# Performance work log

Hardware: AMD Instinct MI355X
Metric: run time of the kernel (lower is better)

Reference implementation:

```python
import jax, jax.numpy as jnp
import numpy as np

D_CH = 2048  # channels
N = 64       # hidden_state
L = 8192     # sequence length
MIN_DELTA, MAX_DELTA = 1e-3, 0.1


def setup_inputs() -> dict:
    key = jax.random.key(0)
    ks = jax.random.split(key, 5)
    X = jax.random.normal(ks[0], (D_CH, L), jnp.float32)
    # kaiming_normal_(nonlinearity='linear'): std = 1/sqrt(fan_in=N)
    A = jax.random.normal(ks[1], (N, N), jnp.float32) * (1.0 / N) ** 0.5
    B = jax.random.normal(ks[2], (N, D_CH), jnp.float32) * (1.0 / N) ** 0.5
    C = jax.random.normal(ks[3], (D_CH, N), jnp.float32)
    Dp = jnp.ones((D_CH,), jnp.float32)
    log_delta = jax.random.uniform(ks[4], (1,), jnp.float32,
                                   float(np.log(MIN_DELTA)), float(np.log(MAX_DELTA)))
    return {"X": X, "A": A, "B": B, "C": C, "Dp": Dp, "log_delta": log_delta}


def reference(X, A, B, C, Dp, log_delta):
    # X: (D, L). Bilinear (Tustin) discretization with dt = exp(log_delta).
    n = A.shape[0]
    delta = jnp.exp(log_delta)[0]
    I = jnp.eye(n, dtype=A.dtype)
    inv = jnp.linalg.inv(I - (delta * 0.5) * A)
    dA = inv @ (I + (delta * 0.5) * A)      # (N, N)
    dB = delta * (inv @ B)                   # (N, D)

    def step(h, x_t):
        # h: (N,), x_t: (D,)
        h = dA @ h + dB @ x_t
        return h, C @ h                      # y_t: (D,)

    h0 = jnp.zeros((n,), X.dtype)
    _, ys = jax.lax.scan(step, h0, X.T)      # ys: (L, D)
    # skip connection y += D * X (per-channel)
    return ys.T + Dp[:, None] * X            # (D, L)
```

## Files before the change

kernel.cpp:

```cpp
#include <hip/hip_runtime.h>
#include <math.h>

#define D_CH 2048
#define LSEQ 8192
#define T1 32
#define NC1 256
#define VSLAB 524288

typedef __attribute__((ext_vector_type(8))) short bf16x8;
typedef __attribute__((ext_vector_type(4))) float f32x4;

__device__ __forceinline__ short f2bf(float x) {
  unsigned u = __float_as_uint(x);
  u += 0x7FFFu + ((u >> 16) & 1);
  return (short)(u >> 16);
}

__device__ __forceinline__ void mmzero(float acc[16]) {
#pragma unroll
  for (int t = 0; t < 16; ++t) acc[t] = 0.f;
}

template <int SZ>
__device__ __forceinline__ void mmld(float acc[16], const float* __restrict__ Z,
                                     int r0, int c0) {
#pragma unroll
  for (int i = 0; i < 4; ++i) {
    float4 z = *(const float4*)&Z[(r0 + i) * SZ + c0];
    acc[i * 4 + 0] = z.x; acc[i * 4 + 1] = z.y;
    acc[i * 4 + 2] = z.z; acc[i * 4 + 3] = z.w;
  }
}

template <int SX, int SY>
__device__ __forceinline__ void mac44(float acc[16], const float* __restrict__ Xb,
                                      const float* __restrict__ Yb, int r0, int c0) {
#pragma unroll 4
  for (int k = 0; k < 64; k += 4) {
    float4 x0 = *(const float4*)&Xb[(r0 + 0) * SX + k];
    float4 x1 = *(const float4*)&Xb[(r0 + 1) * SX + k];
    float4 x2 = *(const float4*)&Xb[(r0 + 2) * SX + k];
    float4 x3 = *(const float4*)&Xb[(r0 + 3) * SX + k];
    float4 y0 = *(const float4*)&Yb[(k + 0) * SY + c0];
    float4 y1 = *(const float4*)&Yb[(k + 1) * SY + c0];
    float4 y2 = *(const float4*)&Yb[(k + 2) * SY + c0];
    float4 y3 = *(const float4*)&Yb[(k + 3) * SY + c0];
#define MROW(i, xi) \
    acc[i * 4 + 0] += xi.x * y0.x + xi.y * y1.x + xi.z * y2.x + xi.w * y3.x; \
    acc[i * 4 + 1] += xi.x * y0.y + xi.y * y1.y + xi.z * y2.y + xi.w * y3.y; \
    acc[i * 4 + 2] += xi.x * y0.z + xi.y * y1.z + xi.z * y2.z + xi.w * y3.z; \
    acc[i * 4 + 3] += xi.x * y0.w + xi.y * y1.w + xi.z * y2.w + xi.w * y3.w;
    MROW(0, x0) MROW(1, x1) MROW(2, x2) MROW(3, x3)
#undef MROW
  }
}

template <int SZ>
__device__ __forceinline__ void mmst(float* Dst, const float acc[16], int r0, int c0) {
#pragma unroll
  for (int i = 0; i < 4; ++i)
    *(float4*)&Dst[(r0 + i) * SZ + c0] =
        make_float4(acc[i * 4 + 0], acc[i * 4 + 1], acc[i * 4 + 2], acc[i * 4 + 3]);
}

__global__ __launch_bounds__(256) void main_kernel(const float* __restrict__ X,
                                                   const float* __restrict__ A,
                                                   const float* __restrict__ B,
                                                   const float* __restrict__ logd,
                                                   float* __restrict__ invdT,
                                                   float* __restrict__ dAg,
                                                   float* __restrict__ V,
                                                   int KS) {
  __shared__ float smem[13056];
  const int tid = threadIdx.x;
  const int lane = tid & 63;
  const int w = tid >> 6;

  if (blockIdx.x == 0) {
    float* b0 = smem;
    float* b1 = smem + 4352;
    float* b2 = smem + 8704;
    const int r0 = (tid >> 4) * 4, c0 = (tid & 15) * 4;
    const float delta = expf(logd[0]);
    const float half = 0.5f * delta;
    float acc[16], acc2[16];

    for (int idx = tid; idx < 4096; idx += 256) {
      int i = idx >> 6, j = idx & 63;
      float p = half * A[idx];
      b0[i * 68 + j] = p;
      b2[i * 68 + j] = p + (i == j ? 1.f : 0.f);
    }
    __syncthreads();
    mmzero(acc); mac44<68, 68>(acc, b0, b0, r0, c0); mmst<68>(b1, acc, r0, c0);
    __syncthreads();
    mmld<68>(acc, b2, r0, c0); mac44<68, 68>(acc, b1, b2, r0, c0);
    mmzero(acc2); mac44<68, 68>(acc2, b1, b1, r0, c0);
    __syncthreads();
    mmst<68>(b0, acc, r0, c0); mmst<68>(b2, acc2, r0, c0);
    __syncthreads();
    mmld<68>(acc, b0, r0, c0); mac44<68, 68>(acc, b2, b0, r0, c0);
    mmzero(acc2); mac44<68, 68>(acc2, b2, b2, r0, c0);
    __syncthreads();
    mmst<68>(b1, acc, r0, c0); mmst<68>(b2, acc2, r0, c0);
    __syncthreads();
    mmld<68>(acc, b1, r0, c0); mac44<68, 68>(acc, b2, b1, r0, c0);
    __syncthreads();
    mmst<68>(b0, acc, r0, c0);
    __syncthreads();

    for (int idx = tid; idx < 4096; idx += 256) {
      int n = idx >> 6, m = idx & 63;
      float qv = b0[n * 68 + m];
      invdT[m * 64 + n] = delta * qv;
      dAg[idx] = 2.f * qv - (n == m ? 1.f : 0.f);
    }
    return;
  }

  const int b = blockIdx.x - 1;
  const int t0 = (b & 127) << 6;
  const int slab = b >> 7;
  const int k0 = slab * KS;
  short* Xs = (short*)smem;
  short* Bs = (short*)smem + 4608;
  const int q = lane >> 4, r = lane & 15;

  f32x4 acc[4];
#pragma unroll
  for (int j = 0; j < 4; ++j) acc[j] = (f32x4){0.f, 0.f, 0.f, 0.f};

  const int brow = (lane >> 3);
  const int bkc = (lane & 7) * 8;

  for (int kk = 0; kk < KS; kk += 64) {
    float xv[16];
    float bv[16];
#pragma unroll
    for (int p = 0; p < 2; ++p)
#pragma unroll
      for (int j = 0; j < 8; ++j)
        xv[p * 8 + j] = X[(size_t)(k0 + kk + p * 32 + w * 8 + j) * LSEQ + t0 + lane];
#pragma unroll
    for (int p = 0; p < 2; ++p) {
      int n = p * 32 + w * 8 + brow;
      float4 f0 = *(const float4*)&B[(size_t)n * D_CH + k0 + kk + bkc];
      float4 f1 = *(const float4*)&B[(size_t)n * D_CH + k0 + kk + bkc + 4];
      bv[p * 8 + 0] = f0.x; bv[p * 8 + 1] = f0.y; bv[p * 8 + 2] = f0.z; bv[p * 8 + 3] = f0.w;
      bv[p * 8 + 4] = f1.x; bv[p * 8 + 5] = f1.y; bv[p * 8 + 6] = f1.z; bv[p * 8 + 7] = f1.w;
    }
    __syncthreads();
#pragma unroll
    for (int p = 0; p < 2; ++p) {
      bf16x8 xp, bp;
#pragma unroll
      for (int j = 0; j < 8; ++j) { xp[j] = f2bf(xv[p * 8 + j]); bp[j] = f2bf(bv[p * 8 + j]); }
      *(bf16x8*)&Xs[lane * 72 + p * 32 + w * 8] = xp;
      *(bf16x8*)&Bs[(p * 32 + w * 8 + brow) * 72 + bkc] = bp;
    }
    __syncthreads();
#pragma unroll
    for (int ks = 0; ks < 64; ks += 32) {
      bf16x8 a = *(const bf16x8*)&Xs[(w * 16 + r) * 72 + ks + q * 8];
#pragma unroll
      for (int j = 0; j < 4; ++j) {
        bf16x8 bb = *(const bf16x8*)&Bs[(j * 16 + r) * 72 + ks + q * 8];
        acc[j] = __builtin_amdgcn_mfma_f32_16x16x32_bf16(a, bb, acc[j], 0, 0, 0);
      }
    }
  }
  float* Vs = V + (size_t)slab * VSLAB;
#pragma unroll
  for (int j = 0; j < 4; ++j)
#pragma unroll
    for (int reg = 0; reg < 4; ++reg)
      Vs[(size_t)(t0 + w * 16 + q * 4 + reg) * 64 + j * 16 + r] = acc[j][reg];
}

__device__ __forceinline__ float matvec(const float ar[64], const float* __restrict__ hb,
                                        float u) {
  float a0 = u, a1 = 0.f, a2 = 0.f, a3 = 0.f;
#pragma unroll
  for (int jj = 0; jj < 64; jj += 4) {
    float4 hv = *(const float4*)&hb[jj];
    a0 += ar[jj + 0] * hv.x;
    a1 += ar[jj + 1] * hv.y;
    a2 += ar[jj + 2] * hv.z;
    a3 += ar[jj + 3] * hv.w;
  }
  return (a0 + a1) + (a2 + a3);
}

__global__ __launch_bounds__(256) void scan1_kernel(const float* __restrict__ V,
                                                    const float* __restrict__ invdT,
                                                    const float* __restrict__ dA,
                                                    float* __restrict__ U,
                                                    float* __restrict__ S,
                                                    float* __restrict__ dA32g,
                                                    float* __restrict__ dA512g,
                                                    int nslab) {
  __shared__ float smem[8704];
  const int tid = threadIdx.x;
  const int c = blockIdx.x;

  if (c == NC1) {
    float* b0 = smem;
    float* b1 = smem + 4352;
    const int r0 = (tid >> 4) * 4, c0 = (tid & 15) * 4;
    for (int idx = tid; idx < 4096; idx += 256)
      b0[(idx >> 6) * 68 + (idx & 63)] = dA[idx];
    __syncthreads();
    float acc[16];
    float* p = b0; float* q = b1;
    for (int s = 1; s <= 9; ++s) {
      mmzero(acc); mac44<68, 68>(acc, p, p, r0, c0);
      if (s == 5) mmst<64>(dA32g, acc, r0, c0);
      if (s == 9) mmst<64>(dA512g, acc, r0, c0);
      mmst<68>(q, acc, r0, c0);
      __syncthreads();
      float* t = p; p = q; q = t;
    }
    return;
  }

  float* invs = smem;
  float* Vs   = smem + 4096;
  float* Us   = smem + 6144;
  float* hs0  = smem + 8192;
  float* hs1  = smem + 8256;

  for (int idx = tid; idx < 4096; idx += 256) invs[idx] = invdT[idx];
  for (int idx = tid; idx < 2048; idx += 256) {
    float v = 0.f;
    for (int s = 0; s < nslab; ++s) v += V[(size_t)s * VSLAB + (size_t)c * 2048 + idx];
    Vs[idx] = v;
  }
  __syncthreads();

  const int r0 = (tid >> 4) * 2, c0 = (tid & 15) * 4;
  float a0[4] = {0.f, 0.f, 0.f, 0.f}, a1[4] = {0.f, 0.f, 0.f, 0.f};
#pragma unroll 4
  for (int k = 0; k < 64; k += 4) {
    float4 v0 = *(const float4*)&Vs[r0 * 64 + k];
    float4 v1 = *(const float4*)&Vs[(r0 + 1) * 64 + k];
    float4 y0 = *(const float4*)&invs[(k + 0) * 64 + c0];
    float4 y1 = *(const float4*)&invs[(k + 1) * 64 + c0];
    float4 y2 = *(const float4*)&invs[(k + 2) * 64 + c0];
    float4 y3 = *(const float4*)&invs[(k + 3) * 64 + c0];
    a0[0] += v0.x * y0.x + v0.y * y1.x + v0.z * y2.x + v0.w * y3.x;
    a0[1] += v0.x * y0.y + v0.y * y1.y + v0.z * y2.y + v0.w * y3.y;
    a0[2] += v0.x * y0.z + v0.y * y1.z + v0.z * y2.z + v0.w * y3.z;
    a0[3] += v0.x * y0.w + v0.y * y1.w + v0.z * y2.w + v0.w * y3.w;
    a1[0] += v1.x * y0.x + v1.y * y1.x + v1.z * y2.x + v1.w * y3.x;
    a1[1] += v1.x * y0.y + v1.y * y1.y + v1.z * y2.y + v1.w * y3.y;
    a1[2] += v1.x * y0.z + v1.y * y1.z + v1.z * y2.z + v1.w * y3.z;
    a1[3] += v1.x * y0.w + v1.y * y1.w + v1.z * y2.w + v1.w * y3.w;
  }
  *(float4*)&Us[r0 * 64 + c0] = make_float4(a0[0], a0[1], a0[2], a0[3]);
  *(float4*)&Us[(r0 + 1) * 64 + c0] = make_float4(a1[0], a1[1], a1[2], a1[3]);
  *(float4*)&U[(size_t)(c * 32 + r0) * 64 + c0] = make_float4(a0[0], a0[1], a0[2], a0[3]);
  *(float4*)&U[(size_t)(c * 32 + r0 + 1) * 64 + c0] = make_float4(a1[0], a1[1], a1[2], a1[3]);
  __syncthreads();

  if (tid < 64) {
    float ar[64];
#pragma unroll
    for (int jj = 0; jj < 64; jj += 4) {
      float4 v = *(const float4*)&dA[tid * 64 + jj];
      ar[jj] = v.x; ar[jj + 1] = v.y; ar[jj + 2] = v.z; ar[jj + 3] = v.w;
    }
    float h = 0.f;
    hs0[tid] = 0.f;
    for (int t = 0; t < T1; ++t) {
      float u = Us[t * 64 + tid];
      h = matvec(ar, (t & 1) ? hs1 : hs0, u);
      ((t & 1) ? hs0 : hs1)[tid] = h;
    }
    S[c * 64 + tid] = h;
  }
}

__global__ __launch_bounds__(1024, 4) void mid_kernel(const float* __restrict__ S,
                                                      const float* __restrict__ dA32,
                                                      const float* __restrict__ dA512,
                                                      float* __restrict__ Hinit) {
  __shared__ float S2s[1024];
  __shared__ float H2s[1024];
  __shared__ float hsbuf[2048];
  const int tid = threadIdx.x;
  const int wave = tid >> 6, lane = tid & 63;
  float* hs0 = &hsbuf[wave * 128];
  float* hs1 = hs0 + 64;
  const float* inw = S + wave * 16 * 64;

  {
    float ar[64];
#pragma unroll
    for (int jj = 0; jj < 64; jj += 4) {
      float4 v = *(const float4*)&dA32[lane * 64 + jj];
      ar[jj] = v.x; ar[jj + 1] = v.y; ar[jj + 2] = v.z; ar[jj + 3] = v.w;
    }
    float h = 0.f;
    hs0[lane] = 0.f;
    for (int t = 0; t < 16; ++t) {
      float u = inw[t * 64 + lane];
      h = matvec(ar, (t & 1) ? hs1 : hs0, u);
      ((t & 1) ? hs0 : hs1)[lane] = h;
    }
    S2s[wave * 64 + lane] = h;
  }
  __syncthreads();

  if (wave == 0) {
    float br[64];
#pragma unroll
    for (int jj = 0; jj < 64; jj += 4) {
      float4 v = *(const float4*)&dA512[lane * 64 + jj];
      br[jj] = v.x; br[jj + 1] = v.y; br[jj + 2] = v.z; br[jj + 3] = v.w;
    }
    float g = 0.f;
    hs0[lane] = 0.f;
    for (int t = 0; t < 16; ++t) {
      H2s[t * 64 + lane] = g;
      float u = S2s[t * 64 + lane];
      g = matvec(br, (t & 1) ? hs1 : hs0, u);
      ((t & 1) ? hs0 : hs1)[lane] = g;
    }
  }
  __syncthreads();

  {
    float ar[64];
#pragma unroll
    for (int jj = 0; jj < 64; jj += 4) {
      float4 v = *(const float4*)&dA32[lane * 64 + jj];
      ar[jj] = v.x; ar[jj + 1] = v.y; ar[jj + 2] = v.z; ar[jj + 3] = v.w;
    }
    float h = H2s[wave * 64 + lane];
    hs0[lane] = h;
    for (int t = 0; t < 16; ++t) {
      Hinit[(wave * 16 + t) * 64 + lane] = h;
      float u = inw[t * 64 + lane];
      h = matvec(ar, (t & 1) ? hs1 : hs0, u);
      ((t & 1) ? hs0 : hs1)[lane] = h;
    }
  }
}

__global__ __launch_bounds__(64) void scan2_kernel(const float* __restrict__ U,
                                                   const float* __restrict__ dA,
                                                   const float* __restrict__ Hinit,
                                                   float* __restrict__ Ht) {
  __shared__ float hs[2][64];
  const int tid = threadIdx.x;
  const int c = blockIdx.x;
  float ar[64];
#pragma unroll
  for (int jj = 0; jj < 64; jj += 4) {
    float4 v = *(const float4*)&dA[tid * 64 + jj];
    ar[jj] = v.x; ar[jj + 1] = v.y; ar[jj + 2] = v.z; ar[jj + 3] = v.w;
  }
  float h = Hinit[c * 64 + tid];
  hs[0][tid] = h;
  const float* inc = U + (size_t)c * T1 * 64;
  float* outc = Ht + (size_t)c * T1 * 64;
  float up[4];
#pragma unroll
  for (int i = 0; i < 4; ++i) up[i] = inc[i * 64 + tid];

  for (int t = 0; t < T1; ++t) {
    float u = up[t & 3];
    if (t + 4 < T1) up[t & 3] = inc[(t + 4) * 64 + tid];
    h = matvec(ar, hs[t & 1], u);
    hs[(t + 1) & 1][tid] = h;
    outc[t * 64 + tid] = h;
  }
}

__global__ __launch_bounds__(256) void out_kernel(const float* __restrict__ X,
                                                  const float* __restrict__ C,
                                                  const float* __restrict__ Dp,
                                                  const float* __restrict__ Ht,
                                                  float* __restrict__ Y) {
  __shared__ short Cs[64 * 72];
  __shared__ short Hs[64 * 72];
  const int tid = threadIdx.x;
  const int lane = tid & 63, w = tid >> 6;
  const int t0 = blockIdx.x * 64;
  const int d0 = blockIdx.y * 64;
  const int q = lane >> 4, r = lane & 15;
  const int brow = lane >> 3, bkc = (lane & 7) * 8;

#pragma unroll
  for (int p = 0; p < 2; ++p) {
    int row = p * 32 + w * 8 + brow;
    float4 c0 = *(const float4*)&C[(size_t)(d0 + row) * 64 + bkc];
    float4 c1 = *(const float4*)&C[(size_t)(d0 + row) * 64 + bkc + 4];
    float4 h0 = *(const float4*)&Ht[(size_t)(t0 + row) * 64 + bkc];
    float4 h1 = *(const float4*)&Ht[(size_t)(t0 + row) * 64 + bkc + 4];
    bf16x8 cv, hv;
    cv[0] = f2bf(c0.x); cv[1] = f2bf(c0.y); cv[2] = f2bf(c0.z); cv[3] = f2bf(c0.w);
    cv[4] = f2bf(c1.x); cv[5] = f2bf(c1.y); cv[6] = f2bf(c1.z); cv[7] = f2bf(c1.w);
    hv[0] = f2bf(h0.x); hv[1] = f2bf(h0.y); hv[2] = f2bf(h0.z); hv[3] = f2bf(h0.w);
    hv[4] = f2bf(h1.x); hv[5] = f2bf(h1.y); hv[6] = f2bf(h1.z); hv[7] = f2bf(h1.w);
    *(bf16x8*)&Cs[row * 72 + bkc] = cv;
    *(bf16x8*)&Hs[row * 72 + bkc] = hv;
  }
  __syncthreads();

  f32x4 acc[4];
#pragma unroll
  for (int j = 0; j < 4; ++j) acc[j] = (f32x4){0.f, 0.f, 0.f, 0.f};
#pragma unroll
  for (int ks = 0; ks < 64; ks += 32) {
    bf16x8 a = *(const bf16x8*)&Cs[(w * 16 + r) * 72 + ks + q * 8];
#pragma unroll
    for (int j = 0; j < 4; ++j) {
      bf16x8 bb = *(const bf16x8*)&Hs[(j * 16 + r) * 72 + ks + q * 8];
      acc[j] = __builtin_amdgcn_mfma_f32_16x16x32_bf16(a, bb, acc[j], 0, 0, 0);
    }
  }

#pragma unroll
  for (int reg = 0; reg < 4; ++reg) {
    int d = d0 + w * 16 + q * 4 + reg;
    float dp = Dp[d];
#pragma unroll
    for (int j = 0; j < 4; ++j) {
      int t = t0 + j * 16 + r;
      size_t off = (size_t)d * LSEQ + t;
      Y[off] = acc[j][reg] + dp * X[off];
    }
  }
}

extern "C" void kernel_launch(void* const* d_in, const int* in_sizes, int n_in,
                              void* d_out, int out_size, void* d_ws, size_t ws_size,
                              hipStream_t stream) {
  const float* X  = (const float*)d_in[0];
  const float* A  = (const float*)d_in[1];
  const float* B  = (const float*)d_in[2];
  const float* Cm = (const float*)d_in[3];
  const float* Dp = (const float*)d_in[4];
  const float* ld = (const float*)d_in[5];
  float* out = (float*)d_out;
  float* ws = (float*)d_ws;

  const size_t need4 = (size_t)(16384 + 4 * VSLAB + VSLAB + 16384 + 16384) * 4;
  const int nslab = (ws_size >= need4) ? 4 : 2;

  float* invdT = ws;
  float* dA    = ws + 4096;
  float* dA32  = ws + 8192;
  float* dA512 = ws + 12288;
  float* V     = ws + 16384;
  float* U     = V + (size_t)nslab * VSLAB;
  float* S     = U + VSLAB;
  float* Hinit = S + 16384;
  float* Ht    = V;

  main_kernel<<<nslab * 128 + 1, 256, 0, stream>>>(X, A, B, ld, invdT, dA, V,
                                                   2048 / nslab);
  scan1_kernel<<<NC1 + 1, 256, 0, stream>>>(V, invdT, dA, U, S, dA32, dA512, nslab);
  mid_kernel<<<1, 1024, 0, stream>>>(S, dA32, dA512, Hinit);
  scan2_kernel<<<NC1, 64, 0, stream>>>(U, dA, Hinit, Ht);
  out_kernel<<<dim3(128, 32), 256, 0, stream>>>(X, Cm, Dp, Ht, out);
}
```

Measured before the change: 255.6 us.

## Halve GEMM time tile, prefetch next K-slice into registers, shrink block-0 LDS

The projection GEMM in main_kernel now uses 32-row time tiles instead of 64, doubling the grid, and splits each block's 32x64 output across four waves in a 2x2 arrangement. Global loads for the next 64-wide K slice are issued right after the LDS stores, so they overlap the MFMA work on the current slice. Block 0's Neumann-series inverse is rewritten as a loop over two LDS buffers, which cuts shared memory from about 52KB to 35KB and may allow more resident blocks. The trade-off is more blocks and redundant B loads per time tile, plus an extra barrier per iteration.

```diff
diff --git a/kernel.cpp b/kernel.cpp
--- a/kernel.cpp
+++ b/kernel.cpp
@@ -71,47 +71,44 @@
                                                    float* __restrict__ dAg,
                                                    float* __restrict__ V,
                                                    int KS) {
-  __shared__ float smem[13056];
+  __shared__ float smem[8704];
   const int tid = threadIdx.x;
   const int lane = tid & 63;
   const int w = tid >> 6;
 
   if (blockIdx.x == 0) {
-    float* b0 = smem;
-    float* b1 = smem + 4352;
-    float* b2 = smem + 8704;
+    float* bQ = smem;
+    float* bP = smem + 4352;
     const int r0 = (tid >> 4) * 4, c0 = (tid & 15) * 4;
     const float delta = expf(logd[0]);
     const float half = 0.5f * delta;
-    float acc[16], acc2[16];
+    float accQ[16], accP[16];
 
     for (int idx = tid; idx < 4096; idx += 256) {
       int i = idx >> 6, j = idx & 63;
       float p = half * A[idx];
-      b0[i * 68 + j] = p;
-      b2[i * 68 + j] = p + (i == j ? 1.f : 0.f);
-    }
-    __syncthreads();
-    mmzero(acc); mac44<68, 68>(acc, b0, b0, r0, c0); mmst<68>(b1, acc, r0, c0);
-    __syncthreads();
-    mmld<68>(acc, b2, r0, c0); mac44<68, 68>(acc, b1, b2, r0, c0);
-    mmzero(acc2); mac44<68, 68>(acc2, b1, b1, r0, c0);
-    __syncthreads();
-    mmst<68>(b0, acc, r0, c0); mmst<68>(b2, acc2, r0, c0);
-    __syncthreads();
-    mmld<68>(acc, b0, r0, c0); mac44<68, 68>(acc, b2, b0, r0, c0);
-    mmzero(acc2); mac44<68, 68>(acc2, b2, b2, r0, c0);
-    __syncthreads();
-    mmst<68>(b1, acc, r0, c0); mmst<68>(b2, acc2, r0, c0);
-    __syncthreads();
-    mmld<68>(acc, b1, r0, c0); mac44<68, 68>(acc, b2, b1, r0, c0);
-    __syncthreads();
-    mmst<68>(b0, acc, r0, c0);
-    __syncthreads();
+      bP[i * 68 + j] = p;
+      bQ[i * 68 + j] = p + (i == j ? 1.f : 0.f);
+    }
+    __syncthreads();
+    mmzero(accP); mac44<68, 68>(accP, bP, bP, r0, c0);
+    __syncthreads();
+    mmst<68>(bP, accP, r0, c0);
+    __syncthreads();
+#pragma unroll 1
+    for (int s = 0; s < 3; ++s) {
+      mmld<68>(accQ, bQ, r0, c0);
+      mac44<68, 68>(accQ, bP, bQ, r0, c0);
+      if (s < 2) { mmzero(accP); mac44<68, 68>(accP, bP, bP, r0, c0); }
+      __syncthreads();
+      mmst<68>(bQ, accQ, r0, c0);
+      if (s < 2) mmst<68>(bP, accP, r0, c0);
+      __syncthreads();
+    }
 
     for (int idx = tid; idx < 4096; idx += 256) {
       int n = idx >> 6, m = idx & 63;
-      float qv = b0[n * 68 + m];
+      float qv = bQ[n * 68 + m];
       invdT[m * 64 + n] = delta * qv;
       dAg[idx] = 2.f * qv - (n == m ? 1.f : 0.f);
     }
@@ -119,62 +116,84 @@
   }
 
   const int b = blockIdx.x - 1;
-  const int t0 = (b & 127) << 6;
-  const int slab = b >> 7;
+  const int t0 = (b & 255) << 5;
+  const int slab = b >> 8;
   const int k0 = slab * KS;
   short* Xs = (short*)smem;
-  short* Bs = (short*)smem + 4608;
+  short* Bs = (short*)smem + 2304;
   const int q = lane >> 4, r = lane & 15;
-
-  f32x4 acc[4];
-#pragma unroll
-  for (int j = 0; j < 4; ++j) acc[j] = (f32x4){0.f, 0.f, 0.f, 0.f};
-
-  const int brow = (lane >> 3);
+  const int hi = lane >> 5, tl = lane & 31;
+  const int brow = lane >> 3;
   const int bkc = (lane & 7) * 8;
+  const int wm = (w & 1) * 16;
+  const int wn = (w >> 1) * 32;
+
+  f32x4 acc[2];
+#pragma unroll
+  for (int j = 0; j < 2; ++j) acc[j] = (f32x4){0.f, 0.f, 0.f, 0.f};
+
+  float xv[8];
+  float bv[16];
+
+#define LOADX(KK)                                                              \
+  _Pragma("unroll")                                                            \
+  for (int j = 0; j < 8; ++j)                                                  \
+    xv[j] = X[(size_t)(k0 + (KK) + w * 16 + hi * 8 + j) * LSEQ + t0 + tl];
+
+#define LOADB(KK)                                                              \
+  _Pragma("unroll")                                                            \
+  for (int p = 0; p < 2; ++p) {                                                \
+    int n = p * 32 + w * 8 + brow;                                             \
+    float4 f0 = *(const float4*)&B[(size_t)n * D_CH + k0 + (KK) + bkc];        \
+    float4 f1 = *(const float4*)&B[(size_t)n * D_CH + k0 + (KK) + bkc + 4];    \
+    bv[p * 8 + 0] = f0.x; bv[p * 8 + 1] = f0.y;                                \
+    bv[p * 8 + 2] = f0.z; bv[p * 8 + 3] = f0.w;                                \
+    bv[p * 8 + 4] = f1.x; bv[p * 8 + 5] = f1.y;                                \
+    bv[p * 8 + 6] = f1.z; bv[p * 8 + 7] = f1.w;                                \
+  }
+
+  LOADX(0)
+  LOADB(0)
 
   for (int kk = 0; kk < KS; kk += 64) {
-    float xv[16];
-    float bv[16];
-#pragma unroll
-    for (int p = 0; p < 2; ++p)
-#pragma unroll
-      for (int j = 0; j < 8; ++j)
-        xv[p * 8 + j] = X[(size_t)(k0 + kk + p * 32 + w * 8 + j) * LSEQ + t0 + lane];
+    bf16x8 xp;
+#pragma unroll
+    for (int j = 0; j < 8; ++j) xp[j] = f2bf(xv[j]);
+    *(bf16x8*)&Xs[tl * 72 + w * 16 + hi * 8] = xp;
 #pragma unroll
     for (int p = 0; p < 2; ++p) {
-      int n = p * 32 + w * 8 + brow;
-      float4 f0 = *(const float4*)&B[(size_t)n * D_CH + k0 + kk + bkc];
-      float4 f1 = *(const float4*)&B[(size_t)n * D_CH + k0 + kk + bkc + 4];
-      bv[p * 8 + 0] = f0.x; bv[p * 8 + 1] = f0.y; bv[p * 8 + 2] = f0.z; bv[p * 8 + 3] = f0.w;
-      bv[p * 8 + 4] = f1.x; bv[p * 8 + 5] = f1.y; bv[p * 8 + 6] = f1.z; bv[p * 8 + 7] = f1.w;
-    }
-    __syncthreads();
-#pragma unroll
-    for (int p = 0; p < 2; ++p) {
-      bf16x8 xp, bp;
-#pragma unroll
-      for (int j = 0; j < 8; ++j) { xp[j] = f2bf(xv[p * 8 + j]); bp[j] = f2bf(bv[p * 8 + j]); }
-      *(bf16x8*)&Xs[lane * 72 + p * 32 + w * 8] = xp;
-      *(bf16x8*)&Bs[(p * 32 + w * 8 + brow) * 72 + bkc] = bp;
-    }
-    __syncthreads();
+      bf16x8 bp8;
+#pragma unroll
+      for (int j = 0; j < 8; ++j) bp8[j] = f2bf(bv[p * 8 + j]);
+      *(bf16x8*)&Bs[(p * 32 + w * 8 + brow) * 72 + bkc] = bp8;
+    }
+    __syncthreads();
+
+    if (kk + 64 < KS) {
+      LOADX(kk + 64)
+      LOADB(kk + 64)
+    }
+
 #pragma unroll
     for (int ks = 0; ks < 64; ks += 32) {
-      bf16x8 a = *(const bf16x8*)&Xs[(w * 16 + r) * 72 + ks + q * 8];
-#pragma unroll
-      for (int j = 0; j < 4; ++j) {
-        bf16x8 bb = *(const bf16x8*)&Bs[(j * 16 + r) * 72 + ks + q * 8];
+      bf16x8 a = *(const bf16x8*)&Xs[(wm + r) * 72 + ks + q * 8];
+#pragma unroll
+      for (int j = 0; j < 2; ++j) {
+        bf16x8 bb = *(const bf16x8*)&Bs[(wn + j * 16 + r) * 72 + ks + q * 8];
         acc[j] = __builtin_amdgcn_mfma_f32_16x16x32_bf16(a, bb, acc[j], 0, 0, 0);
       }
     }
-  }
+    __syncthreads();
+  }
+#undef LOADX
+#undef LOADB
+
   float* Vs = V + (size_t)slab * VSLAB;
 #pragma unroll
-  for (int j = 0; j < 4; ++j)
+  for (int j = 0; j < 2; ++j)
 #pragma unroll
     for (int reg = 0; reg < 4; ++reg)
-      Vs[(size_t)(t0 + w * 16 + q * 4 + reg) * 64 + j * 16 + r] = acc[j][reg];
+      Vs[(size_t)(t0 + wm + q * 4 + reg) * 64 + wn + j * 16 + r] = acc[j][reg];
 }
 
 __device__ __forceinline__ float matvec(const float ar[64], const float* __restrict__ hb,
@@ -459,7 +478,7 @@
   float* Hinit = S + 16384;
   float* Ht    = V;
 
-  main_kernel<<<nslab * 128 + 1, 256, 0, stream>>>(X, A, B, ld, invdT, dA, V,
+  main_kernel<<<nslab * 256 + 1, 256, 0, stream>>>(X, A, B, ld, invdT, dA, V,
                                                    2048 / nslab);
   scan1_kernel<<<NC1 + 1, 256, 0, stream>>>(V, invdT, dA, U, S, dA32, dA512, nslab);
   mid_kernel<<<1, 1024, 0, stream>>>(S, dA32, dA512, Hinit);
```

Result: no change. 257.1 us (+0.6%).
